# Performance work log

Hardware: AMD Instinct MI355X
Metric: run time of the kernel (lower is better)

## Reference

```python
import jax, jax.numpy as jnp
import numpy as np


def setup_inputs() -> dict:
    key = jax.random.key(0)
    kx, ka, kw, kb = jax.random.split(key, 4)
    B, N, IN, OUT = 4, 4096, 128, 128
    X = jax.random.normal(kx, (B, N, IN), dtype=jnp.float32)
    A = jax.random.uniform(ka, (B, N, N), dtype=jnp.float32)
    # nn.Linear(in_dim, out_dim): W is [out_dim, in_dim], b is [out_dim]
    bound = 1.0 / np.sqrt(IN)
    W = jax.random.uniform(kw, (OUT, IN), dtype=jnp.float32, minval=-bound, maxval=bound)
    b = jax.random.uniform(kb, (OUT,), dtype=jnp.float32, minval=-bound, maxval=bound)
    return {"X": X, "A": A, "W": W, "b": b}


def reference(X, A, W, b):
    B, N, _ = X.shape
    # A_hat = A + I (self loops)
    A_hat = A + jnp.eye(N, dtype=A.dtype)[None, :, :]
    deg = A_hat.sum(-1)  # [B, N]
    d_inv_sqrt = jnp.where(deg > 0, jax.lax.rsqrt(deg), 0.0)  # inf -> 0 as in torch code
    # D^{-1/2} A_hat D^{-1/2}: diag bmms are row/col scaling (same math, no N^3 diag GEMMs)
    A_norm = d_inv_sqrt[:, :, None] * A_hat * d_inv_sqrt[:, None, :]
    H = jnp.einsum('bnm,bmd->bnd', A_norm, X)  # propagation
    return jnp.einsum('bnd,od->bno', H, W) + b  # linear
```

## Files before the change

### kernel.cpp

```cpp
#include <hip/hip_runtime.h>
#include <hip/hip_bf16.h>
#include <stdint.h>

#define BB 4
#define NN 4096
#define DD 128

typedef __attribute__((ext_vector_type(8))) short short8;
typedef __attribute__((ext_vector_type(4))) float f32x4;

static __device__ __forceinline__ unsigned short f2bf(float f) {
  unsigned u = __builtin_bit_cast(unsigned, f);
  u += 0x7fffu + ((u >> 16) & 1u);
  return (unsigned short)(u >> 16);
}
static __device__ __forceinline__ float bf2f(unsigned short s) {
  return __builtin_bit_cast(float, (unsigned)s << 16);
}

__global__ __launch_bounds__(256) void k_deg(const float* __restrict__ A,
                                             float* __restrict__ dinv) {
  const int row = blockIdx.x;
  const float* a = A + (size_t)row * NN;
  float s = 0.f;
  for (int i = threadIdx.x * 4; i < NN; i += 256 * 4) {
    const float4 v = *reinterpret_cast<const float4*>(a + i);
    s += (v.x + v.y) + (v.z + v.w);
  }
  for (int off = 32; off > 0; off >>= 1) s += __shfl_down(s, off, 64);
  __shared__ float red[4];
  if ((threadIdx.x & 63) == 0) red[threadIdx.x >> 6] = s;
  __syncthreads();
  if (threadIdx.x == 0) {
    const float deg = (red[0] + red[1]) + (red[2] + red[3]) + 1.0f;
    dinv[row] = 1.0f / sqrtf(deg);
  }
}

__global__ __launch_bounds__(256) void k_prep(const float* __restrict__ X,
                                              const float* __restrict__ dinv,
                                              unsigned short* __restrict__ Yt,
                                              unsigned short* __restrict__ Yr)
{
  __shared__ unsigned short tile[64][130];
  const int b = blockIdx.x >> 6;
  const int m0 = (blockIdx.x & 63) << 6;
  const float* Xb = X + ((size_t)b * NN + m0) * DD;
  const float* dv = dinv + b * NN + m0;
  for (int idx = threadIdx.x; idx < 64 * 128; idx += 256) {
    const int mi = idx >> 7, d = idx & 127;
    const unsigned short u = f2bf(Xb[mi * DD + d] * dv[mi]);
    tile[mi][d] = u;
    Yr[((size_t)b * NN + m0 + mi) * DD + d] = u;
  }
  __syncthreads();
  for (int idx = threadIdx.x; idx < 128 * 64; idx += 256) {
    const int d = idx >> 6, j = idx & 63;
    Yt[((size_t)b * DD + d) * NN + m0 + j] = tile[j][d];
  }
}

__global__ __launch_bounds__(256) void k_w(const float* __restrict__ W,
                                           unsigned short* __restrict__ Wb) {
  int idx = blockIdx.x * 1024 + threadIdx.x;
  for (int k = 0; k < 4; ++k, idx += 256) Wb[idx] = f2bf(W[idx]);
}

__global__ __launch_bounds__(512) void k_main(const float* __restrict__ A,
                                              const unsigned short* __restrict__ Yt,
                                              const unsigned short* __restrict__ Yr,
                                              const float* __restrict__ dinv,
                                              unsigned short* __restrict__ Hb) {
  __shared__ char lds[49152];

  const int tid = threadIdx.x;
  const int l   = tid & 63;
  const int wid = tid >> 6;
  const int b   = blockIdx.x >> 6;
  const int n0  = (blockIdx.x & 63) << 6;
  const int wr  = wid >> 2;
  const int wc  = wid & 3;

  const float* Ab = A + (size_t)(b * NN + n0) * NN;
  const unsigned short* Ytb = Yt + (size_t)b * DD * NN;

  const int sar = tid >> 3;
  const int sac = (tid & 7) << 3;
  const float* pA = Ab + (size_t)sar * NN + sac;
  const int awb = sar * 128 + (((tid & 7) << 4) ^ ((sar & 7) << 4));

  const int brow_i0 = wid * 16 + (l >> 3);
  const int bg      = ((l & 7) ^ (l >> 3)) << 3;
  const char* pB0 = (const char*)(Ytb + (size_t)brow_i0 * NN + bg);
  const char* pB1 = (const char*)(Ytb + (size_t)(brow_i0 + 8) * NN + bg);

  float4 ra0, ra1;
  auto LOADA = [&](int t) {
    ra0 = *reinterpret_cast<const float4*>(pA + t * 64);
    ra1 = *reinterpret_cast<const float4*>(pA + t * 64 + 4);
  };
  auto CVTWRITEA = [&](int nb) {
    short8 v;
    v[0] = (short)f2bf(ra0.x); v[1] = (short)f2bf(ra0.y);
    v[2] = (short)f2bf(ra0.z); v[3] = (short)f2bf(ra0.w);
    v[4] = (short)f2bf(ra1.x); v[5] = (short)f2bf(ra1.y);
    v[6] = (short)f2bf(ra1.z); v[7] = (short)f2bf(ra1.w);
    *reinterpret_cast<short8*>(lds + nb * 24576 + awb) = v;
  };
  auto GLDSB = [&](int t, int nb) {
    char* dst = lds + nb * 24576 + 8192 + (wid * 2) * 1024;
    __builtin_amdgcn_global_load_lds(pB0 + (size_t)t * 128, dst, 16, 0, 0);
    __builtin_amdgcn_global_load_lds(pB1 + (size_t)t * 128, dst + 1024, 16, 0, 0);
  };

  f32x4 acc[2][2] = {};
  const int lrow = l & 15;
  const int lg   = l >> 4;
  const int ar0 = wr * 32 + lrow, ar1 = ar0 + 16;
  const int br0 = wc * 32 + lrow, br1 = br0 + 16;

  auto COMPUTE = [&](int nb) {
    const char* Abase = lds + nb * 24576;
    const char* Bbase = Abase + 8192;
#pragma unroll
    for (int kc = 0; kc < 2; ++kc) {
      const int g = kc * 4 + lg;
      const short8 a0 = *reinterpret_cast<const short8*>(Abase + ar0 * 128 + ((g ^ (ar0 & 7)) << 4));
      const short8 a1 = *reinterpret_cast<const short8*>(Abase + ar1 * 128 + ((g ^ (ar1 & 7)) << 4));
      const short8 b0 = *reinterpret_cast<const short8*>(Bbase + br0 * 128 + ((g ^ (br0 & 7)) << 4));
      const short8 b1 = *reinterpret_cast<const short8*>(Bbase + br1 * 128 + ((g ^ (br1 & 7)) << 4));
      acc[0][0] = __builtin_amdgcn_mfma_f32_16x16x32_bf16(a0, b0, acc[0][0], 0, 0, 0);
      acc[0][1] = __builtin_amdgcn_mfma_f32_16x16x32_bf16(a0, b1, acc[0][1], 0, 0, 0);
      acc[1][0] = __builtin_amdgcn_mfma_f32_16x16x32_bf16(a1, b0, acc[1][0], 0, 0, 0);
      acc[1][1] = __builtin_amdgcn_mfma_f32_16x16x32_bf16(a1, b1, acc[1][1], 0, 0, 0);
    }
  };

  LOADA(0);
  GLDSB(0, 0);
  asm volatile("s_waitcnt vmcnt(2)" ::: "memory");
  CVTWRITEA(0);
  LOADA(1);
  GLDSB(1, 1);
  asm volatile("s_waitcnt vmcnt(4) lgkmcnt(0)" ::: "memory");
  __builtin_amdgcn_s_barrier();

  const int NT = NN / 64;
  for (int t = 0; t < NT; ++t) {
    COMPUTE(t & 1);
    __builtin_amdgcn_s_barrier();
    if (t + 1 < NT) {
      asm volatile("s_waitcnt vmcnt(2)" ::: "memory");
      CVTWRITEA((t + 1) & 1);
      if (t + 2 < NT) {
        LOADA(t + 2);
        GLDSB(t + 2, t & 1);
        asm volatile("s_waitcnt vmcnt(4) lgkmcnt(0)" ::: "memory");
      } else {
        asm volatile("s_waitcnt vmcnt(0) lgkmcnt(0)" ::: "memory");
      }
      __builtin_amdgcn_s_barrier();
    }
  }

  const int rg = lg << 2;
#pragma unroll
  for (int mi = 0; mi < 2; ++mi)
#pragma unroll
    for (int ni = 0; ni < 2; ++ni)
#pragma unroll
      for (int r = 0; r < 4; ++r) {
        const int n = n0 + wr * 32 + mi * 16 + rg + r;
        const int d = wc * 32 + ni * 16 + lrow;
        const size_t gi = (size_t)(b * NN + n) * DD + d;
        const float h = (acc[mi][ni][r] + bf2f(Yr[gi])) * dinv[b * NN + n];
        Hb[gi] = f2bf(h);
      }
}

__global__ __launch_bounds__(512) void k_lin(const unsigned short* __restrict__ Hb,
                                             const unsigned short* __restrict__ Wb,
                                             const float* __restrict__ bias,
                                             float* __restrict__ out) {
  __shared__ char lds[49152];

  const int tid = threadIdx.x;
  const int l   = tid & 63;
  const int wid = tid >> 6;
  const int wr  = wid >> 2;
  const int wc  = wid & 3;
  const size_t r0 = (size_t)blockIdx.x * 64;

#pragma unroll
  for (int i = 0; i < 2; ++i) {
    const int c = tid + i * 512;
    const int row = c >> 4, colb = (c & 15) << 4;
    const uint4 v = *reinterpret_cast<const uint4*>(Hb + (r0 + row) * DD + (colb >> 1));
    *reinterpret_cast<uint4*>(lds + row * 256 + (colb ^ ((row & 7) << 4))) = v;
  }
#pragma unroll
  for (int i = 0; i < 4; ++i) {
    const int c = tid + i * 512;
    const int row = c >> 4, colb = (c & 15) << 4;
    const uint4 v = *reinterpret_cast<const uint4*>(Wb + row * DD + (colb >> 1));
    *reinterpret_cast<uint4*>(lds + 16384 + row * 256 + (colb ^ ((row & 7) << 4))) = v;
  }
  __syncthreads();

  f32x4 acc[2][2] = {};
  const int lrow = l & 15;
  const int lk16 = (l >> 4) << 4;
  const int arow0 = wr * 32 + lrow, arow1 = arow0 + 16;
  const int brow0 = wc * 32 + lrow, brow1 = brow0 + 16;
#pragma unroll
  for (int ks = 0; ks < 4; ++ks) {
    const int kb = ks * 64 + lk16;
    const short8 a0 = *reinterpret_cast<const short8*>(lds + arow0 * 256 + (kb ^ ((arow0 & 7) << 4)));
    const short8 a1 = *reinterpret_cast<const short8*>(lds + arow1 * 256 + (kb ^ ((arow1 & 7) << 4)));
    const short8 b0 = *reinterpret_cast<const short8*>(lds + 16384 + brow0 * 256 + (kb ^ ((brow0 & 7) << 4)));
    const short8 b1 = *reinterpret_cast<const short8*>(lds + 16384 + brow1 * 256 + (kb ^ ((brow1 & 7) << 4)));
    acc[0][0] = __builtin_amdgcn_mfma_f32_16x16x32_bf16(a0, b0, acc[0][0], 0, 0, 0);
    acc[0][1] = __builtin_amdgcn_mfma_f32_16x16x32_bf16(a0, b1, acc[0][1], 0, 0, 0);
    acc[1][0] = __builtin_amdgcn_mfma_f32_16x16x32_bf16(a1, b0, acc[1][0], 0, 0, 0);
    acc[1][1] = __builtin_amdgcn_mfma_f32_16x16x32_bf16(a1, b1, acc[1][1], 0, 0, 0);
  }

  const int rg = (l >> 4) << 2;
#pragma unroll
  for (int mi = 0; mi < 2; ++mi)
#pragma unroll
    for (int ni = 0; ni < 2; ++ni) {
      const int o = wc * 32 + ni * 16 + lrow;
      const float bo = bias[o];
#pragma unroll
      for (int r = 0; r < 4; ++r) {
        const int nloc = wr * 32 + mi * 16 + rg + r;
        out[(r0 + nloc) * DD + o] = acc[mi][ni][r] + bo;
      }
    }
}

extern "C" void kernel_launch(void* const* d_in, const int* in_sizes, int n_in,
                              void* d_out, int out_size, void* d_ws, size_t ws_size,
                              hipStream_t stream) {
  const float* X    = (const float*)d_in[0];
  const float* A    = (const float*)d_in[1];
  const float* W    = (const float*)d_in[2];
  const float* bias = (const float*)d_in[3];
  float* out = (float*)d_out;

  char* ws = (char*)d_ws;
  float* dinv = (float*)ws;
  unsigned short* Yt = (unsigned short*)(ws + 65536);
  unsigned short* Yr = Yt + (size_t)BB * DD * NN;
  unsigned short* Hb = Yr + (size_t)BB * NN * DD;
  unsigned short* Wb = Hb + (size_t)BB * NN * DD;

  k_deg <<<BB * NN, 256, 0, stream>>>(A, dinv);
  k_w   <<<16, 256, 0, stream>>>(W, Wb);
  k_prep<<<BB * (NN / 64), 256, 0, stream>>>(X, dinv, Yt, Yr);
  k_main<<<BB * (NN / 64), 512, 0, stream>>>(A, Yt, Yr, dinv, Hb);
  k_lin <<<(BB * NN) / 64, 512, 0, stream>>>(Hb, Wb, bias, out);
}
```

Baseline: 122.1 us.

## Fuse linear layer into propagation kernel and widen K tile to 128

Merges the final linear GEMM and bias into the main propagation kernel. H is staged in LDS as bf16 and multiplied by W there, so the Hb round trip and the separate k_lin launch go away. The self-loop term now reads X in fp32 directly instead of a separate bf16 Yr copy, which removes Yr from k_prep. The K tile doubles from 64 to 128, with a new pipeline and 96KB of LDS per block. The larger LDS footprint may lower occupancy, and the pipeline does a redundant last-tile load.

```diff
diff --git a/kernel.cpp b/kernel.cpp
--- a/kernel.cpp
+++ b/kernel.cpp
@@ -5,6 +5,7 @@
 #define BB 4
 #define NN 4096
 #define DD 128
+#define BK 128
 
 typedef __attribute__((ext_vector_type(8))) short short8;
 typedef __attribute__((ext_vector_type(4))) float f32x4;
@@ -13,9 +14,6 @@
   unsigned u = __builtin_bit_cast(unsigned, f);
   u += 0x7fffu + ((u >> 16) & 1u);
   return (unsigned short)(u >> 16);
-}
-static __device__ __forceinline__ float bf2f(unsigned short s) {
-  return __builtin_bit_cast(float, (unsigned)s << 16);
 }
 
 __global__ __launch_bounds__(256) void k_deg(const float* __restrict__ A,
@@ -39,9 +37,7 @@
 
 __global__ __launch_bounds__(256) void k_prep(const float* __restrict__ X,
                                               const float* __restrict__ dinv,
-                                              unsigned short* __restrict__ Yt,
-                                              unsigned short* __restrict__ Yr)
-{
+                                              unsigned short* __restrict__ Yt) {
   __shared__ unsigned short tile[64][130];
   const int b = blockIdx.x >> 6;
   const int m0 = (blockIdx.x & 63) << 6;
@@ -49,9 +45,7 @@
   const float* dv = dinv + b * NN + m0;
   for (int idx = threadIdx.x; idx < 64 * 128; idx += 256) {
     const int mi = idx >> 7, d = idx & 127;
-    const unsigned short u = f2bf(Xb[mi * DD + d] * dv[mi]);
-    tile[mi][d] = u;
-    Yr[((size_t)b * NN + m0 + mi) * DD + d] = u;
+    tile[mi][d] = f2bf(Xb[mi * DD + d] * dv[mi]);
   }
   __syncthreads();
   for (int idx = threadIdx.x; idx < 128 * 64; idx += 256) {
@@ -68,10 +62,12 @@
 
 __global__ __launch_bounds__(512) void k_main(const float* __restrict__ A,
                                               const unsigned short* __restrict__ Yt,
-                                              const unsigned short* __restrict__ Yr,
+                                              const unsigned short* __restrict__ Wb,
+                                              const float* __restrict__ X,
                                               const float* __restrict__ dinv,
-                                              unsigned short* __restrict__ Hb) {
-  __shared__ char lds[49152];
+                                              const float* __restrict__ bias,
+                                              float* __restrict__ out) {
+  __shared__ char lds[98304];
 
   const int tid = threadIdx.x;
   const int l   = tid & 63;
@@ -85,159 +81,121 @@
   const unsigned short* Ytb = Yt + (size_t)b * DD * NN;
 
   const int sar = tid >> 3;
-  const int sac = (tid & 7) << 3;
-  const float* pA = Ab + (size_t)sar * NN + sac;
-  const int awb = sar * 128 + (((tid & 7) << 4) ^ ((sar & 7) << 4));
-
-  const int brow_i0 = wid * 16 + (l >> 3);
-  const int bg      = ((l & 7) ^ (l >> 3)) << 3;
-  const char* pB0 = (const char*)(Ytb + (size_t)brow_i0 * NN + bg);
-  const char* pB1 = (const char*)(Ytb + (size_t)(brow_i0 + 8) * NN + bg);
-
-  float4 ra0, ra1;
+  const int sg0 = (tid & 7) << 1;
+  const float* pA = Ab + (size_t)sar * NN + (sg0 << 3);
+  float4 ra[4];
   auto LOADA = [&](int t) {
-    ra0 = *reinterpret_cast<const float4*>(pA + t * 64);
-    ra1 = *reinterpret_cast<const float4*>(pA + t * 64 + 4);
-  };
-  auto CVTWRITEA = [&](int nb) {
-    short8 v;
-    v[0] = (short)f2bf(ra0.x); v[1] = (short)f2bf(ra0.y);
-    v[2] = (short)f2bf(ra0.z); v[3] = (short)f2bf(ra0.w);
-    v[4] = (short)f2bf(ra1.x); v[5] = (short)f2bf(ra1.y);
-    v[6] = (short)f2bf(ra1.z); v[7] = (short)f2bf(ra1.w);
-    *reinterpret_cast<short8*>(lds + nb * 24576 + awb) = v;
-  };
-  auto GLDSB = [&](int t, int nb) {
-    char* dst = lds + nb * 24576 + 8192 + (wid * 2) * 1024;
-    __builtin_amdgcn_global_load_lds(pB0 + (size_t)t * 128, dst, 16, 0, 0);
-    __builtin_amdgcn_global_load_lds(pB1 + (size_t)t * 128, dst + 1024, 16, 0, 0);
-  };
-
-  f32x4 acc[2][2] = {};
+#pragma unroll
+    for (int i = 0; i < 4; ++i)
+      ra[i] = *reinterpret_cast<const float4*>(pA + t * BK + i * 4);
+  };
+  auto CVTA = [&](int nb) {
+    char* As = lds + nb * 49152 + sar * 256;
+#pragma unroll
+    for (int j = 0; j < 2; ++j) {
+      short8 v;
+      v[0] = (short)f2bf(ra[2*j].x);   v[1] = (short)f2bf(ra[2*j].y);
+      v[2] = (short)f2bf(ra[2*j].z);   v[3] = (short)f2bf(ra[2*j].w);
+      v[4] = (short)f2bf(ra[2*j+1].x); v[5] = (short)f2bf(ra[2*j+1].y);
+      v[6] = (short)f2bf(ra[2*j+1].z); v[7] = (short)f2bf(ra[2*j+1].w);
+      *reinterpret_cast<short8*>(As + (((sg0 + j) ^ (sar & 15)) << 4)) = v;
+    }
+  };
+
+  const int glrow4 = l >> 4;
+  const int glslot = l & 15;
+  auto GLDS = [&](const unsigned short* src, int rstride, int colh, char* dstBase) {
+#pragma unroll
+    for (int i = 0; i < 4; ++i) {
+      const int rloc = wid * 16 + i * 4 + glrow4;
+      const int g = glslot ^ ((i * 4 + glrow4) & 15);
+      __builtin_amdgcn_global_load_lds(src + (size_t)rloc * rstride + colh + g * 8,
+                                       dstBase + (wid * 16 + i * 4) * 256, 16, 0, 0);
+    }
+  };
+
   const int lrow = l & 15;
   const int lg   = l >> 4;
   const int ar0 = wr * 32 + lrow, ar1 = ar0 + 16;
   const int br0 = wc * 32 + lrow, br1 = br0 + 16;
 
-  auto COMPUTE = [&](int nb) {
-    const char* Abase = lds + nb * 24576;
-    const char* Bbase = Abase + 8192;
-#pragma unroll
-    for (int kc = 0; kc < 2; ++kc) {
+  f32x4 acc[2][2] = {};
+  auto GEMMSTEP = [&](int nb, f32x4 (&ac)[2][2]) {
+    const char* Ap = lds + nb * 49152;
+    const char* Bp = Ap + 16384;
+#pragma unroll
+    for (int kc = 0; kc < 4; ++kc) {
       const int g = kc * 4 + lg;
-      const short8 a0 = *reinterpret_cast<const short8*>(Abase + ar0 * 128 + ((g ^ (ar0 & 7)) << 4));
-      const short8 a1 = *reinterpret_cast<const short8*>(Abase + ar1 * 128 + ((g ^ (ar1 & 7)) << 4));
-      const short8 b0 = *reinterpret_cast<const short8*>(Bbase + br0 * 128 + ((g ^ (br0 & 7)) << 4));
-      const short8 b1 = *reinterpret_cast<const short8*>(Bbase + br1 * 128 + ((g ^ (br1 & 7)) << 4));
-      acc[0][0] = __builtin_amdgcn_mfma_f32_16x16x32_bf16(a0, b0, acc[0][0], 0, 0, 0);
-      acc[0][1] = __builtin_amdgcn_mfma_f32_16x16x32_bf16(a0, b1, acc[0][1], 0, 0, 0);
-      acc[1][0] = __builtin_amdgcn_mfma_f32_16x16x32_bf16(a1, b0, acc[1][0], 0, 0, 0);
-      acc[1][1] = __builtin_amdgcn_mfma_f32_16x16x32_bf16(a1, b1, acc[1][1], 0, 0, 0);
+      const short8 a0 = *reinterpret_cast<const short8*>(Ap + ar0 * 256 + ((g ^ (ar0 & 15)) << 4));
+      const short8 a1 = *reinterpret_cast<const short8*>(Ap + ar1 * 256 + ((g ^ (ar1 & 15)) << 4));
+      const short8 b0 = *reinterpret_cast<const short8*>(Bp + br0 * 256 + ((g ^ (br0 & 15)) << 4));
+      const short8 b1 = *reinterpret_cast<const short8*>(Bp + br1 * 256 + ((g ^ (br1 & 15)) << 4));
+      ac[0][0] = __builtin_amdgcn_mfma_f32_16x16x32_bf16(a0, b0, ac[0][0], 0, 0, 0);
+      ac[0][1] = __builtin_amdgcn_mfma_f32_16x16x32_bf16(a0, b1, ac[0][1], 0, 0, 0);
+      ac[1][0] = __builtin_amdgcn_mfma_f32_16x16x32_bf16(a1, b0, ac[1][0], 0, 0, 0);
+      ac[1][1] = __builtin_amdgcn_mfma_f32_16x16x32_bf16(a1, b1, ac[1][1], 0, 0, 0);
     }
   };
 
   LOADA(0);
-  GLDSB(0, 0);
-  asm volatile("s_waitcnt vmcnt(2)" ::: "memory");
-  CVTWRITEA(0);
+  GLDS(Ytb, NN, 0, lds + 16384);
+  asm volatile("s_waitcnt vmcnt(4)" ::: "memory");
+  CVTA(0);
   LOADA(1);
-  GLDSB(1, 1);
-  asm volatile("s_waitcnt vmcnt(4) lgkmcnt(0)" ::: "memory");
+  GLDS(Ytb, NN, BK, lds + 49152 + 16384);
+  asm volatile("s_waitcnt vmcnt(8) lgkmcnt(0)" ::: "memory");
   __builtin_amdgcn_s_barrier();
 
-  const int NT = NN / 64;
+  const int NT = NN / BK;
   for (int t = 0; t < NT; ++t) {
-    COMPUTE(t & 1);
+    const int cur = t & 1;
+    asm volatile("s_waitcnt vmcnt(4)" ::: "memory");
+    CVTA(cur ^ 1);
+    GEMMSTEP(cur, acc);
+    asm volatile("s_waitcnt vmcnt(0) lgkmcnt(0)" ::: "memory");
     __builtin_amdgcn_s_barrier();
-    if (t + 1 < NT) {
-      asm volatile("s_waitcnt vmcnt(2)" ::: "memory");
-      CVTWRITEA((t + 1) & 1);
-      if (t + 2 < NT) {
-        LOADA(t + 2);
-        GLDSB(t + 2, t & 1);
-        asm volatile("s_waitcnt vmcnt(4) lgkmcnt(0)" ::: "memory");
-      } else {
-        asm volatile("s_waitcnt vmcnt(0) lgkmcnt(0)" ::: "memory");
+    const int tn = (t + 2 < NT) ? t + 2 : NT - 1;
+    LOADA(tn);
+    GLDS(Ytb, NN, tn * BK, lds + cur * 49152 + 16384);
+  }
+
+  const int rg = lg << 2;
+  const float* Xb  = X + (size_t)(b * NN + n0) * DD;
+  const float* dvb = dinv + b * NN + n0;
+#pragma unroll
+  for (int mi = 0; mi < 2; ++mi)
+#pragma unroll
+    for (int r = 0; r < 4; ++r) {
+      const int nl = wr * 32 + mi * 16 + rg + r;
+      const float dn = dvb[nl];
+#pragma unroll
+      for (int ni = 0; ni < 2; ++ni) {
+        const int d = wc * 32 + ni * 16 + lrow;
+        const float h = dn * (acc[mi][ni][r] + dn * Xb[nl * DD + d]);
+        *reinterpret_cast<unsigned short*>(
+            lds + nl * 256 + (((d >> 3) ^ (nl & 15)) << 4) + (d & 7) * 2) = f2bf(h);
       }
-      __builtin_amdgcn_s_barrier();
-    }
-  }
-
-  const int rg = lg << 2;
-#pragma unroll
-  for (int mi = 0; mi < 2; ++mi)
-#pragma unroll
-    for (int ni = 0; ni < 2; ++ni)
+    }
+  GLDS(Wb, DD, 0, lds + 16384);
+  asm volatile("s_waitcnt vmcnt(0) lgkmcnt(0)" ::: "memory");
+  __builtin_amdgcn_s_barrier();
+
+  f32x4 acc2[2][2] = {};
+  GEMMSTEP(0, acc2);
+
+  float* outb = out + (size_t)(b * NN + n0) * DD;
+#pragma unroll
+  for (int ni = 0; ni < 2; ++ni) {
+    const int o = wc * 32 + ni * 16 + lrow;
+    const float bo = bias[o];
+#pragma unroll
+    for (int mi = 0; mi < 2; ++mi)
 #pragma unroll
       for (int r = 0; r < 4; ++r) {
-        const int n = n0 + wr * 32 + mi * 16 + rg + r;
-        const int d = wc * 32 + ni * 16 + lrow;
-        const size_t gi = (size_t)(b * NN + n) * DD + d;
-        const float h = (acc[mi][ni][r] + bf2f(Yr[gi])) * dinv[b * NN + n];
-        Hb[gi] = f2bf(h);
+        const int nl = wr * 32 + mi * 16 + rg + r;
+        outb[(size_t)nl * DD + o] = acc2[mi][ni][r] + bo;
       }
-}
-
-__global__ __launch_bounds__(512) void k_lin(const unsigned short* __restrict__ Hb,
-                                             const unsigned short* __restrict__ Wb,
-                                             const float* __restrict__ bias,
-                                             float* __restrict__ out) {
-  __shared__ char lds[49152];
-
-  const int tid = threadIdx.x;
-  const int l   = tid & 63;
-  const int wid = tid >> 6;
-  const int wr  = wid >> 2;
-  const int wc  = wid & 3;
-  const size_t r0 = (size_t)blockIdx.x * 64;
-
-#pragma unroll
-  for (int i = 0; i < 2; ++i) {
-    const int c = tid + i * 512;
-    const int row = c >> 4, colb = (c & 15) << 4;
-    const uint4 v = *reinterpret_cast<const uint4*>(Hb + (r0 + row) * DD + (colb >> 1));
-    *reinterpret_cast<uint4*>(lds + row * 256 + (colb ^ ((row & 7) << 4))) = v;
-  }
-#pragma unroll
-  for (int i = 0; i < 4; ++i) {
-    const int c = tid + i * 512;
-    const int row = c >> 4, colb = (c & 15) << 4;
-    const uint4 v = *reinterpret_cast<const uint4*>(Wb + row * DD + (colb >> 1));
-    *reinterpret_cast<uint4*>(lds + 16384 + row * 256 + (colb ^ ((row & 7) << 4))) = v;
-  }
-  __syncthreads();
-
-  f32x4 acc[2][2] = {};
-  const int lrow = l & 15;
-  const int lk16 = (l >> 4) << 4;
-  const int arow0 = wr * 32 + lrow, arow1 = arow0 + 16;
-  const int brow0 = wc * 32 + lrow, brow1 = brow0 + 16;
-#pragma unroll
-  for (int ks = 0; ks < 4; ++ks) {
-    const int kb = ks * 64 + lk16;
-    const short8 a0 = *reinterpret_cast<const short8*>(lds + arow0 * 256 + (kb ^ ((arow0 & 7) << 4)));
-    const short8 a1 = *reinterpret_cast<const short8*>(lds + arow1 * 256 + (kb ^ ((arow1 & 7) << 4)));
-    const short8 b0 = *reinterpret_cast<const short8*>(lds + 16384 + brow0 * 256 + (kb ^ ((brow0 & 7) << 4)));
-    const short8 b1 = *reinterpret_cast<const short8*>(lds + 16384 + brow1 * 256 + (kb ^ ((brow1 & 7) << 4)));
-    acc[0][0] = __builtin_amdgcn_mfma_f32_16x16x32_bf16(a0, b0, acc[0][0], 0, 0, 0);
-    acc[0][1] = __builtin_amdgcn_mfma_f32_16x16x32_bf16(a0, b1, acc[0][1], 0, 0, 0);
-    acc[1][0] = __builtin_amdgcn_mfma_f32_16x16x32_bf16(a1, b0, acc[1][0], 0, 0, 0);
-    acc[1][1] = __builtin_amdgcn_mfma_f32_16x16x32_bf16(a1, b1, acc[1][1], 0, 0, 0);
-  }
-
-  const int rg = (l >> 4) << 2;
-#pragma unroll
-  for (int mi = 0; mi < 2; ++mi)
-#pragma unroll
-    for (int ni = 0; ni < 2; ++ni) {
-      const int o = wc * 32 + ni * 16 + lrow;
-      const float bo = bias[o];
-#pragma unroll
-      for (int r = 0; r < 4; ++r) {
-        const int nloc = wr * 32 + mi * 16 + rg + r;
-        out[(r0 + nloc) * DD + o] = acc[mi][ni][r] + bo;
-      }
-    }
+  }
 }
 
 extern "C" void kernel_launch(void* const* d_in, const int* in_sizes, int n_in,
@@ -252,13 +210,10 @@
   char* ws = (char*)d_ws;
   float* dinv = (float*)ws;
   unsigned short* Yt = (unsigned short*)(ws + 65536);
-  unsigned short* Yr = Yt + (size_t)BB * DD * NN;
-  unsigned short* Hb = Yr + (size_t)BB * NN * DD;
-  unsigned short* Wb = Hb + (size_t)BB * NN * DD;
+  unsigned short* Wb = Yt + (size_t)BB * DD * NN;
 
   k_deg <<<BB * NN, 256, 0, stream>>>(A, dinv);
   k_w   <<<16, 256, 0, stream>>>(W, Wb);
-  k_prep<<<BB * (NN / 64), 256, 0, stream>>>(X, dinv, Yt, Yr);
-  k_main<<<BB * (NN / 64), 512, 0, stream>>>(A, Yt, Yr, dinv, Hb);
-  k_lin <<<(BB * NN) / 64, 512, 0, stream>>>(Hb, Wb, bias, out);
-}
+  k_prep<<<BB * (NN / 64), 256, 0, stream>>>(X, dinv, Yt);
+  k_main<<<BB * (NN / 64), 512, 0, stream>>>(A, Yt, Wb, X, dinv, bias, out);
+}
```

Result: no change. 122.9 us (+0.7%).
